# Optimization experiments

Measured on AMD Instinct MI355X. Metric: run time of the kernel, lower is better.

## Reference

```python
import jax, jax.numpy as jnp
import numpy as np

NF, NH1, NH21, NH22, NCLS = 6, 128, 128, 128, 3
OBS_X, OBS_Y, OBS_Z, R = 10.0, 10.0, 9.0, 7.0
BATCH = 131072


def setup_inputs() -> dict:
    key = jax.random.key(0)
    ks = jax.random.split(key, 16)
    def lin(kw, kb, fan_in, fan_out):
        bound = 1.0 / np.sqrt(fan_in)
        w = jax.random.uniform(kw, (fan_out, fan_in), jnp.float32, -bound, bound)
        b = jax.random.uniform(kb, (fan_out,), jnp.float32, -bound, bound)
        return w, b
    fc1_w, fc1_b = lin(ks[0], ks[1], NF, NH1)
    fc21_w, fc21_b = lin(ks[2], ks[3], NH1, NH21)
    fc22_w, fc22_b = lin(ks[4], ks[5], NH1, NH22)
    fcm1_w, fcm1_b = lin(ks[6], ks[7], NH21, NH21)
    fcm2_w, fcm2_b = lin(ks[8], ks[9], NH22, NH22)
    fc31_w, fc31_b = lin(ks[10], ks[11], NH21, NCLS)
    fc32_w, fc32_b = lin(ks[12], ks[13], NH22, 2)
    x = jax.random.normal(ks[14], (BATCH, NF), jnp.float32)
    mean = jnp.array([10.0, 0.0, 10.0, 0.0, 9.0, 0.0], jnp.float32)
    std = jnp.array([5.0, 2.0, 5.0, 2.0, 5.0, 2.0], jnp.float32)
    return {"x": x, "mean": mean, "std": std,
            "fc1_w": fc1_w, "fc1_b": fc1_b,
            "fc21_w": fc21_w, "fc21_b": fc21_b,
            "fc22_w": fc22_w, "fc22_b": fc22_b,
            "fcm1_w": fcm1_w, "fcm1_b": fcm1_b,
            "fcm2_w": fcm2_w, "fcm2_b": fcm2_b,
            "fc31_w": fc31_w, "fc31_b": fc31_b,
            "fc32_w": fc32_w, "fc32_b": fc32_b,
            "sgn": 1}


def _forward(x, mean, std, fc1_w, fc1_b, fc21_w, fc21_b, fc22_w, fc22_b,
             fcm1_w, fcm1_b, fcm2_w, fcm2_b, fc31_w, fc31_b, fc32_w, fc32_b):
    x0 = x * std + mean                                   # de-normalized state [B,6]
    h = jnp.tanh(x @ fc1_w.T + fc1_b)                     # [B,NH1]
    x21 = jnp.tanh(h @ fc21_w.T + fc21_b)
    x22 = jnp.tanh(h @ fc22_w.T + fc22_b)
    x21 = jnp.tanh(x21 @ fcm1_w.T + fcm1_b)
    x22 = jnp.tanh(x22 @ fcm2_w.T + fcm2_b)
    x31 = x21 @ fc31_w.T + fc31_b                         # QP linear term p, [B,3]
    x32 = 4.0 * jax.nn.sigmoid(x22 @ fc32_w.T + fc32_b)   # HOCBF penalties, [B,2]

    # higher-order CBF terms
    px, vx, py, vy, pz, vz = (x0[:, i] for i in range(6))
    dx, dy, dz = px - OBS_X, py - OBS_Y, pz - OBS_Z
    barrier = dx**4 + dy**4 + dz**4 - R**4
    barrier_dot = 4.0 * (dx**3 * vx + dy**3 * vy + dz**3 * vz)
    Lf2b = 12.0 * (dx**2 * vx**2 + dy**2 * vy**2 + dz**2 * vz**2)
    G = -4.0 * jnp.stack([dx**3, dy**3, dz**3], axis=-1)  # [B,3], single constraint G u <= h
    hvec = Lf2b + (x32[:, 0] + x32[:, 1]) * barrier_dot + x32[:, 0] * x32[:, 1] * barrier  # [B]

    # QP: min 0.5 u^T u + x31^T u  s.t.  G u <= h  (Q = I, one constraint)
    # Closed-form KKT: u = -x31 - lam*G, lam = max(0, (G @ (-x31) - h) / (G @ G))
    u_unc = -x31
    Gu = jnp.sum(G * u_unc, axis=-1)                      # [B]
    GG = jnp.sum(G * G, axis=-1)                          # [B]
    lam = jnp.maximum(Gu - hvec, 0.0) / GG
    u = u_unc - lam[:, None] * G                          # [B,3]
    return u


def reference(x, mean, std, fc1_w, fc1_b, fc21_w, fc21_b, fc22_w, fc22_b,
              fcm1_w, fcm1_b, fcm2_w, fcm2_b, fc31_w, fc31_b, fc32_w, fc32_b, sgn):
    return _forward(x, mean, std, fc1_w, fc1_b, fc21_w, fc21_b, fc22_w, fc22_b,
                    fcm1_w, fcm1_b, fcm2_w, fcm2_b, fc31_w, fc31_b, fc32_w, fc32_b)
```

## Files before the change

kernel.cpp:

```cpp
#include <hip/hip_runtime.h>

typedef _Float16 half8 __attribute__((ext_vector_type(8)));
typedef _Float16 half4_t __attribute__((ext_vector_type(4)));
typedef __fp16 fp16x2 __attribute__((ext_vector_type(2)));
typedef float float4_t __attribute__((ext_vector_type(4)));
typedef float float2_t __attribute__((ext_vector_type(2)));
typedef float float16_t __attribute__((ext_vector_type(16)));

#define SB 64
#define NT 512
#define RS (SB * 8)

#define OFF_W1   0
#define OFF_W21  4096
#define OFF_W22  20480
#define OFF_WM1  36864
#define OFF_WM2  53248
#define OFF_W4A  69632
#define OFF_BIAS 73728
#define WS_HELEMS 73728

#define SCL_TANH 2.8853900817779268f
#define SCL_SIG  -1.4426950408889634f

__device__ __forceinline__ float tanh_pre(float a) {
  float e = __builtin_amdgcn_exp2f(a);
  return fmaf(-2.f, __builtin_amdgcn_rcpf(1.f + e), 1.f);
}
__device__ __forceinline__ half4_t pack4(float v0, float v1, float v2, float v3) {
  fp16x2 lo = __builtin_amdgcn_cvt_pkrtz(v0, v1);
  fp16x2 hi = __builtin_amdgcn_cvt_pkrtz(v2, v3);
  half4_t h;
  h[0] = (_Float16)lo[0]; h[1] = (_Float16)lo[1];
  h[2] = (_Float16)hi[0]; h[3] = (_Float16)hi[1];
  return h;
}

__global__ void prepack(const float* __restrict__ w1, const float* __restrict__ w21,
                        const float* __restrict__ w22, const float* __restrict__ wm1,
                        const float* __restrict__ wm2, const float* __restrict__ w31,
                        const float* __restrict__ w32, const float* __restrict__ b1,
                        const float* __restrict__ b21, const float* __restrict__ b22,
                        const float* __restrict__ bm1, const float* __restrict__ bm2,
                        _Float16* __restrict__ ws) {
  const int stride = gridDim.x * blockDim.x;
  for (int i = blockIdx.x * blockDim.x + threadIdx.x; i < WS_HELEMS; i += stride) {
    float v;
    if (i < OFF_W21) {
      int j = i & 7, c = i >> 3, m32 = c & 31, t1 = c >> 5;
      int half = t1 & 1, t2 = t1 >> 1, kc = t2 & 1, mt = t2 >> 1;
      int row = mt * 32 + m32, k = kc * 16 + half * 8 + j;
      v = (k < 6) ? w1[row * 6 + k] * SCL_TANH : 0.f;
    } else if (i < OFF_W4A) {
      int t = i - OFF_W21;
      int m = t >> 14; t &= 16383;
      const float* src = (m == 0) ? w21 : (m == 1) ? w22 : (m == 2) ? wm1 : wm2;
      int j = t & 7, c = t >> 3, m32 = c & 31, t1 = c >> 5;
      int half = t1 & 1, t2 = t1 >> 1, kc = t2 & 7, mt = t2 >> 3;
      v = src[(mt * 32 + m32) * 128 + kc * 16 + half * 8 + j] * SCL_TANH;
    } else if (i < OFF_BIAS) {
      int t = i - OFF_W4A;
      int j = t & 7, r = t >> 3, l16 = r & 15, q = r >> 4;
      int cc = q & 15, chain = q >> 4;
      int k = cc * 8 + j, m = l16;
      if (chain == 0) v = (m < 3) ? w31[m * 128 + k] : 0.f;
      else            v = (m < 2) ? w32[m * 128 + k] * SCL_SIG : 0.f;
    } else { v = 0.f; }
    ws[i] = (_Float16)v;
  }
  float* bws = (float*)(ws + OFF_BIAS);
  for (int i = blockIdx.x * blockDim.x + threadIdx.x; i < 640; i += stride) {
    int layer = i >> 7, idx = i & 127;
    const float* src = (layer == 0) ? b1 : (layer == 1) ? b21
                     : (layer == 2) ? b22 : (layer == 3) ? bm1 : bm2;
    bws[i] = src[idx] * SCL_TANH;
  }
}

template <int KC>
__device__ __forceinline__ void loadA32(half8* A, const _Float16* base,
                                        int mt, int half, int m32) {
#pragma unroll
  for (int kc = 0; kc < KC; ++kc)
    A[kc] = *(const half8*)(base + (((mt * KC + kc) * 2 + half) * 32 + m32) * 8);
}

__device__ __forceinline__ float16_t bias_init32(const float* biasL, int mt, int half) {
  float16_t a;
#pragma unroll
  for (int G = 0; G < 4; ++G) {
    float4_t bv = *(const float4_t*)(biasL + mt * 32 + G * 8 + 4 * half);
#pragma unroll
    for (int i2 = 0; i2 < 4; ++i2) a[G * 4 + i2] = bv[i2];
  }
  return a;
}

__device__ __forceinline__ void store32(float16_t acc, _Float16* outB,
                                        int mt, int half, int sOff) {
#pragma unroll
  for (int G = 0; G < 4; ++G) {
    half4_t h = pack4(tanh_pre(acc[G * 4 + 0]), tanh_pre(acc[G * 4 + 1]),
                      tanh_pre(acc[G * 4 + 2]), tanh_pre(acc[G * 4 + 3]));
    *(half4_t*)(outB + (mt * 4 + G) * RS + sOff * 8 + 4 * half) = h;
  }
}

__device__ __forceinline__ void pass32(const half8* A, const float* biasL,
                                       const _Float16* inB, _Float16* outB,
                                       int mt, int half, int sOff) {
  float16_t acc = bias_init32(biasL, mt, half);
#pragma unroll
  for (int kc = 0; kc < 8; ++kc) {
    half8 b = *(const half8*)(inB + (kc * 2 + half) * RS + sOff * 8);
    acc = __builtin_amdgcn_mfma_f32_32x32x16_f16(A[kc], b, acc, 0, 0, 0);
  }
  store32(acc, outB, mt, half, sOff);
}

__global__ __launch_bounds__(NT, 4) void bnet_main(
    const float* __restrict__ x, const float* __restrict__ meang,
    const float* __restrict__ stdg, const float* __restrict__ b31,
    const float* __restrict__ b32, const _Float16* __restrict__ ws,
    float* __restrict__ out) {
  __shared__ __align__(16) _Float16 bufH[SB * 128];
  __shared__ __align__(16) _Float16 bufA[SB * 128];
  __shared__ __align__(16) _Float16 bufB[SB * 128];

  const int tid = threadIdx.x;
  const int wv = tid >> 6;
  const int lane = tid & 63;
  const int half = lane >> 5;
  const int m32 = lane & 31;
  const int mt = wv & 3;
  const int sg = wv >> 2;
  const int sOff = sg * 32 + m32;
  const int quad = lane >> 4;
  const int l16 = lane & 15;
  const int s0 = blockIdx.x * SB;
  const float* biasF = (const float*)(ws + OFF_BIAS);

  half8 A21[8], A22[8];
  loadA32<8>(A21, ws + OFF_W21, mt, half, m32);
  loadA32<8>(A22, ws + OFF_W22, mt, half, m32);

  {
    float16_t acc = bias_init32(biasF, mt, half);
    half8 v;
#pragma unroll
    for (int j = 0; j < 8; ++j) v[j] = (_Float16)0.f;
    if (half == 0) {
      const float* xp = x + (size_t)(s0 + sOff) * 6;
      float2_t e0 = *(const float2_t*)(xp);
      float2_t e1 = *(const float2_t*)(xp + 2);
      float2_t e2 = *(const float2_t*)(xp + 4);
      v[0] = (_Float16)e0[0]; v[1] = (_Float16)e0[1];
      v[2] = (_Float16)e1[0]; v[3] = (_Float16)e1[1];
      v[4] = (_Float16)e2[0]; v[5] = (_Float16)e2[1];
    }
    half8 A1 = *(const half8*)(ws + OFF_W1 + ((mt * 2 * 2 + half) * 32 + m32) * 8);
    acc = __builtin_amdgcn_mfma_f32_32x32x16_f16(A1, v, acc, 0, 0, 0);
    store32(acc, bufH, mt, half, sOff);
  }
  __syncthreads();

  {
    float16_t a1 = bias_init32(biasF + 128, mt, half);
    float16_t a2 = bias_init32(biasF + 256, mt, half);
#pragma unroll
    for (int kc = 0; kc < 8; ++kc) {
      half8 b = *(const half8*)(bufH + (kc * 2 + half) * RS + sOff * 8);
      a1 = __builtin_amdgcn_mfma_f32_32x32x16_f16(A21[kc], b, a1, 0, 0, 0);
      a2 = __builtin_amdgcn_mfma_f32_32x32x16_f16(A22[kc], b, a2, 0, 0, 0);
    }
    store32(a1, bufA, mt, half, sOff);
    store32(a2, bufB, mt, half, sOff);
  }
  half8 AM1[8];
  loadA32<8>(AM1, ws + OFF_WM1, mt, half, m32);
  __syncthreads();

  pass32(AM1, biasF + 384, bufA, bufH, mt, half, sOff);
  half8 AM2[8];
  loadA32<8>(AM2, ws + OFF_WM2, mt, half, m32);
  half8 A4[2][4];
  if (wv < 4) {
#pragma unroll
    for (int c = 0; c < 2; ++c)
#pragma unroll
      for (int kk = 0; kk < 4; ++kk)
        A4[c][kk] = *(const half8*)(ws + OFF_W4A +
                                    ((c * 16 + kk * 4 + quad) * 16 + l16) * 8);
  }
  __syncthreads();

  pass32(AM2, biasF + 512, bufB, bufA, mt, half, sOff);
  float4_t c0 = (float4_t){0.f, 0.f, 0.f, 0.f};
  if (wv < 4) {
    if (quad == 0) { c0[0] = b31[0]; c0[1] = b31[1]; c0[2] = b31[2]; }
    const int nt = wv;
#pragma unroll
    for (int kk = 0; kk < 4; ++kk) {
      half8 bh = *(const half8*)(bufH + (kk * 4 + quad) * RS + (nt * 16 + l16) * 8);
      c0 = __builtin_amdgcn_mfma_f32_16x16x32_f16(A4[0][kk], bh, c0, 0, 0, 0);
    }
  }
  __syncthreads();

  if (wv < 4) {
    const int nt = wv;
    float4_t c1 = (float4_t){0.f, 0.f, 0.f, 0.f};
    if (quad == 0) { c1[0] = b32[0] * SCL_SIG; c1[1] = b32[1] * SCL_SIG; }
#pragma unroll
    for (int kk = 0; kk < 4; ++kk) {
      half8 bc = *(const half8*)(bufA + (kk * 4 + quad) * RS + (nt * 16 + l16) * 8);
      c1 = __builtin_amdgcn_mfma_f32_16x16x32_f16(A4[1][kk], bc, c1, 0, 0, 0);
    }
    if (quad == 0) {
      const int s = nt * 16 + l16;
      float u0 = -c0[0];
      float u1 = -c0[1];
      float u2 = -c0[2];
      float p0 = 4.f * __builtin_amdgcn_rcpf(1.f + __builtin_amdgcn_exp2f(c1[0]));
      float p1 = 4.f * __builtin_amdgcn_rcpf(1.f + __builtin_amdgcn_exp2f(c1[1]));
      const float m0 = meang[0], m1 = meang[1], m2 = meang[2];
      const float m3 = meang[3], m4 = meang[4], m5 = meang[5];
      const float sd0 = stdg[0], sd1 = stdg[1], sd2 = stdg[2];
      const float sd3 = stdg[3], sd4 = stdg[4], sd5 = stdg[5];
      const float* xp = x + (size_t)(s0 + s) * 6;
      float2_t e0 = *(const float2_t*)(xp);
      float2_t e1 = *(const float2_t*)(xp + 2);
      float2_t e2 = *(const float2_t*)(xp + 4);
      float px = e0[0] * sd0 + m0, vx = e0[1] * sd1 + m1;
      float py = e1[0] * sd2 + m2, vy = e1[1] * sd3 + m3;
      float pz = e2[0] * sd4 + m4, vz = e2[1] * sd5 + m5;
      float dx = px - 10.f, dy = py - 10.f, dz = pz - 9.f;
      float dx2 = dx * dx, dy2 = dy * dy, dz2 = dz * dz;
      float dx3 = dx2 * dx, dy3 = dy2 * dy, dz3 = dz2 * dz;
      float barrier = dx3 * dx + dy3 * dy + dz3 * dz - 2401.f;
      float bdot = 4.f * (dx3 * vx + dy3 * vy + dz3 * vz);
      float Lf2b = 12.f * (dx2 * vx * vx + dy2 * vy * vy + dz2 * vz * vz);
      float g0 = -4.f * dx3, g1 = -4.f * dy3, g2 = -4.f * dz3;
      float hv = Lf2b + (p0 + p1) * bdot + p0 * p1 * barrier;
      float Gu = g0 * u0 + g1 * u1 + g2 * u2;
      float GG = g0 * g0 + g1 * g1 + g2 * g2;
      float lam = fmaxf(Gu - hv, 0.f) / GG;
      float* op = out + (size_t)(s0 + s) * 3;
      op[0] = u0 - lam * g0;
      op[1] = u1 - lam * g1;
      op[2] = u2 - lam * g2;
    }
  }
}

extern "C" void kernel_launch(void* const* d_in, const int* in_sizes, int n_in,
                              void* d_out, int out_size, void* d_ws, size_t ws_size,
                              hipStream_t stream) {
  const float* x    = (const float*)d_in[0];
  const float* mean = (const float*)d_in[1];
  const float* stdv = (const float*)d_in[2];
  const float* w1   = (const float*)d_in[3];
  const float* b1   = (const float*)d_in[4];
  const float* w21  = (const float*)d_in[5];
  const float* b21  = (const float*)d_in[6];
  const float* w22  = (const float*)d_in[7];
  const float* b22  = (const float*)d_in[8];
  const float* wm1  = (const float*)d_in[9];
  const float* bm1  = (const float*)d_in[10];
  const float* wm2  = (const float*)d_in[11];
  const float* bm2  = (const float*)d_in[12];
  const float* w31  = (const float*)d_in[13];
  const float* b31  = (const float*)d_in[14];
  const float* w32  = (const float*)d_in[15];
  const float* b32  = (const float*)d_in[16];
  _Float16* ws = (_Float16*)d_ws;
  float* out = (float*)d_out;
  const int batch = in_sizes[0] / 6;

  hipLaunchKernelGGL(prepack, dim3(96), dim3(256), 0, stream,
                     w1, w21, w22, wm1, wm2, w31, w32,
                     b1, b21, b22, bm1, bm2, ws);
  hipLaunchKernelGGL(bnet_main, dim3(batch / SB), dim3(NT), 0, stream,
                     x, mean, stdv, b31, b32, (const _Float16*)ws, out);
}
```

Measured before the change: 127.9 us.

## Recompute first layer per wave to drop a barrier, fold its bias, split MFMA chains

Each wave now computes all four row tiles of the first layer for its own samples. That makes the block barrier between layer 1 and the fc21/fc22 layer unnecessary, at the cost of redundant MFMAs and duplicate LDS writes. The fc1 bias is folded into the weight matrix through a constant 1 input column, so it is rounded to fp16. The remaining biases are repacked so each lane loads its slice contiguously, and are preloaded into registers. The two hidden-to-hidden passes split the K loop across two independent accumulators to shorten MFMA dependency chains, which raises register pressure.

After: 143.7 us. +12.4%, slower.

```diff
diff --git a/kernel.cpp b/kernel.cpp
--- a/kernel.cpp
+++ b/kernel.cpp
@@ -50,7 +50,8 @@
       int j = i & 7, c = i >> 3, m32 = c & 31, t1 = c >> 5;
       int half = t1 & 1, t2 = t1 >> 1, kc = t2 & 1, mt = t2 >> 1;
       int row = mt * 32 + m32, k = kc * 16 + half * 8 + j;
-      v = (k < 6) ? w1[row * 6 + k] * SCL_TANH : 0.f;
+      v = (k < 6) ? w1[row * 6 + k] * SCL_TANH
+        : (k == 6) ? b1[row] * SCL_TANH : 0.f;
     } else if (i < OFF_W4A) {
       int t = i - OFF_W21;
       int m = t >> 14; t &= 16383;
@@ -69,11 +70,14 @@
     ws[i] = (_Float16)v;
   }
   float* bws = (float*)(ws + OFF_BIAS);
-  for (int i = blockIdx.x * blockDim.x + threadIdx.x; i < 640; i += stride) {
-    int layer = i >> 7, idx = i & 127;
-    const float* src = (layer == 0) ? b1 : (layer == 1) ? b21
-                     : (layer == 2) ? b22 : (layer == 3) ? bm1 : bm2;
-    bws[i] = src[idx] * SCL_TANH;
+  for (int i = blockIdx.x * blockDim.x + threadIdx.x; i < 512; i += stride) {
+    int layer = i >> 7, r = i & 127;
+    int mt = r >> 5, rest = r & 31, half = rest >> 4, t = rest & 15;
+    int G = t >> 2, e = t & 3;
+    int row = mt * 32 + G * 8 + 4 * half + e;
+    const float* src = (layer == 0) ? b21 : (layer == 1) ? b22
+                     : (layer == 2) ? bm1 : bm2;
+    bws[i] = src[row] * SCL_TANH;
   }
 }
 
@@ -85,13 +89,13 @@
     A[kc] = *(const half8*)(base + (((mt * KC + kc) * 2 + half) * 32 + m32) * 8);
 }
 
-__device__ __forceinline__ float16_t bias_init32(const float* biasL, int mt, int half) {
+__device__ __forceinline__ float16_t ld_bias16(const float* p) {
   float16_t a;
 #pragma unroll
   for (int G = 0; G < 4; ++G) {
-    float4_t bv = *(const float4_t*)(biasL + mt * 32 + G * 8 + 4 * half);
-#pragma unroll
-    for (int i2 = 0; i2 < 4; ++i2) a[G * 4 + i2] = bv[i2];
+    float4_t v = *(const float4_t*)(p + G * 4);
+#pragma unroll
+    for (int e = 0; e < 4; ++e) a[G * 4 + e] = v[e];
   }
   return a;
 }
@@ -106,16 +110,23 @@
   }
 }
 
-__device__ __forceinline__ void pass32(const half8* A, const float* biasL,
-                                       const _Float16* inB, _Float16* outB,
-                                       int mt, int half, int sOff) {
-  float16_t acc = bias_init32(biasL, mt, half);
-#pragma unroll
-  for (int kc = 0; kc < 8; ++kc) {
-    half8 b = *(const half8*)(inB + (kc * 2 + half) * RS + sOff * 8);
-    acc = __builtin_amdgcn_mfma_f32_32x32x16_f16(A[kc], b, acc, 0, 0, 0);
-  }
-  store32(acc, outB, mt, half, sOff);
+__device__ __forceinline__ void passM(const half8* A, float16_t binit,
+                                      const _Float16* inB, _Float16* outB,
+                                      int mt, int half, int sOff) {
+  float16_t aa = binit;
+  float16_t ab;
+#pragma unroll
+  for (int i = 0; i < 16; ++i) ab[i] = 0.f;
+#pragma unroll
+  for (int kc = 0; kc < 4; ++kc) {
+    half8 b0 = *(const half8*)(inB + (kc * 2 + half) * RS + sOff * 8);
+    half8 b1v = *(const half8*)(inB + ((kc + 4) * 2 + half) * RS + sOff * 8);
+    aa = __builtin_amdgcn_mfma_f32_32x32x16_f16(A[kc], b0, aa, 0, 0, 0);
+    ab = __builtin_amdgcn_mfma_f32_32x32x16_f16(A[kc + 4], b1v, ab, 0, 0, 0);
+  }
+#pragma unroll
+  for (int i = 0; i < 16; ++i) aa[i] += ab[i];
+  store32(aa, outB, mt, half, sOff);
 }
 
 __global__ __launch_bounds__(NT, 4) void bnet_main(
@@ -139,13 +150,15 @@
   const int l16 = lane & 15;
   const int s0 = blockIdx.x * SB;
   const float* biasF = (const float*)(ws + OFF_BIAS);
-
+  const int bb = (mt * 2 + half) * 16;
+
+  float16_t B21r = ld_bias16(biasF + 0 * 128 + bb);
+  float16_t B22r = ld_bias16(biasF + 1 * 128 + bb);
   half8 A21[8], A22[8];
   loadA32<8>(A21, ws + OFF_W21, mt, half, m32);
   loadA32<8>(A22, ws + OFF_W22, mt, half, m32);
 
   {
-    float16_t acc = bias_init32(biasF, mt, half);
     half8 v;
 #pragma unroll
     for (int j = 0; j < 8; ++j) v[j] = (_Float16)0.f;
@@ -157,16 +170,25 @@
       v[0] = (_Float16)e0[0]; v[1] = (_Float16)e0[1];
       v[2] = (_Float16)e1[0]; v[3] = (_Float16)e1[1];
       v[4] = (_Float16)e2[0]; v[5] = (_Float16)e2[1];
-    }
-    half8 A1 = *(const half8*)(ws + OFF_W1 + ((mt * 2 * 2 + half) * 32 + m32) * 8);
-    acc = __builtin_amdgcn_mfma_f32_32x32x16_f16(A1, v, acc, 0, 0, 0);
-    store32(acc, bufH, mt, half, sOff);
-  }
-  __syncthreads();
+      v[6] = (_Float16)1.f;
+    }
+    float16_t z;
+#pragma unroll
+    for (int i = 0; i < 16; ++i) z[i] = 0.f;
+#pragma unroll
+    for (int mtl = 0; mtl < 4; ++mtl) {
+      half8 A1 = *(const half8*)(ws + OFF_W1 + (((mtl * 2) * 2 + half) * 32 + m32) * 8);
+      float16_t acc = __builtin_amdgcn_mfma_f32_32x32x16_f16(A1, v, z, 0, 0, 0);
+      store32(acc, bufH, mtl, half, sOff);
+    }
+  }
+
+  float16_t BM1r = ld_bias16(biasF + 2 * 128 + bb);
+  half8 AM1[8];
+  loadA32<8>(AM1, ws + OFF_WM1, mt, half, m32);
 
   {
-    float16_t a1 = bias_init32(biasF + 128, mt, half);
-    float16_t a2 = bias_init32(biasF + 256, mt, half);
+    float16_t a1 = B21r, a2 = B22r;
 #pragma unroll
     for (int kc = 0; kc < 8; ++kc) {
       half8 b = *(const half8*)(bufH + (kc * 2 + half) * RS + sOff * 8);
@@ -176,11 +198,10 @@
     store32(a1, bufA, mt, half, sOff);
     store32(a2, bufB, mt, half, sOff);
   }
-  half8 AM1[8];
-  loadA32<8>(AM1, ws + OFF_WM1, mt, half, m32);
   __syncthreads();
 
-  pass32(AM1, biasF + 384, bufA, bufH, mt, half, sOff);
+  passM(AM1, BM1r, bufA, bufH, mt, half, sOff);
+  float16_t BM2r = ld_bias16(biasF + 3 * 128 + bb);
   half8 AM2[8];
   loadA32<8>(AM2, ws + OFF_WM2, mt, half, m32);
   half8 A4[2][4];
@@ -194,7 +215,7 @@
   }
   __syncthreads();
 
-  pass32(AM2, biasF + 512, bufB, bufA, mt, half, sOff);
+  passM(AM2, BM2r, bufB, bufA, mt, half, sOff);
   float4_t c0 = (float4_t){0.f, 0.f, 0.f, 0.f};
   if (wv < 4) {
     if (quad == 0) { c0[0] = b31[0]; c0[1] = b31[1]; c0[2] = b31[2]; }
```
